# Kernel tuning notes

Hardware: AMD Instinct MI355X
Metric: run time of the kernel (lower is better)

The kernel has to match this reference:

```python
import jax, jax.numpy as jnp
import numpy as np

B, Q, D, E, V, K = 128, 32, 512, 300, 50000, 21

def kernel_mus(n):
    mus = [1.0]
    if n == 1:
        return mus
    bin_size = 2.0 / (n - 1)
    mus.append(1 - bin_size / 2)
    for i in range(1, n - 1):
        mus.append(mus[i] - bin_size)
    return mus

def kernel_sigmas(n):
    if n == 1:
        return [0.001]
    return [0.001] + [0.1] * (n - 1)

MU = jnp.asarray(kernel_mus(K), dtype=jnp.float32)        # (K,)
SIGMA = jnp.asarray(kernel_sigmas(K), dtype=jnp.float32)  # (K,)

def setup_inputs() -> dict:
    key = jax.random.key(0)
    k1, k2, k3, k4, k5, k6, k7 = jax.random.split(key, 7)
    query_idx = jax.random.randint(k1, (B, Q), 0, V)
    doc_idx = jax.random.randint(k2, (B, D), 0, V)
    query_len = jax.random.randint(k3, (B,), 1, Q + 1)
    doc_len = jax.random.randint(k4, (B,), 1, D + 1)
    emb_table = jax.random.normal(k5, (V, E), dtype=jnp.float32) * 0.1
    dense_w = jax.random.normal(k6, (1, K), dtype=jnp.float32) * 0.1
    dense_b = jax.random.normal(k7, (1,), dtype=jnp.float32) * 0.1
    return {"query_idx": query_idx, "doc_idx": doc_idx,
            "query_len": query_len, "doc_len": doc_len,
            "emb_table": emb_table, "dense_w": dense_w, "dense_b": dense_b}

def _l2norm(x):
    # F.normalize(x, p=2, dim=2): x / max(||x||, 1e-12)
    n = jnp.sqrt(jnp.sum(x * x, axis=-1, keepdims=True))
    return x / jnp.maximum(n, 1e-12)

def reference(query_idx, doc_idx, query_len, doc_len, emb_table, dense_w, dense_b):
    q_embed = _l2norm(emb_table[query_idx])   # (B,Q,E)
    d_embed = _l2norm(emb_table[doc_idx])     # (B,D,E)
    mask_q = (jnp.arange(Q)[None, :] < query_len[:, None]).astype(jnp.float32)  # (B,Q)
    mask_d = (jnp.arange(D)[None, :] < doc_len[:, None]).astype(jnp.float32)    # (B,D)
    sim = jnp.einsum('bqe,bde->bqd', q_embed, d_embed)  # (B,Q,D)
    # Gaussian kernel pooling: (B,Q,D,K) broadcast
    diff = sim[..., None] - MU
    pooling = jnp.exp(-(diff * diff) / (2.0 * SIGMA * SIGMA)) * mask_d[:, None, :, None]
    pooling_sum = jnp.sum(pooling, axis=2)                      # (B,Q,K)
    log_pool = jnp.log(jnp.clip(pooling_sum, 1e-10)) * mask_q[..., None] * 0.01
    log_pooling_sum = jnp.sum(log_pool, axis=1)                 # (B,K)
    score = jnp.squeeze(log_pooling_sum @ dense_w.T + dense_b, axis=1)  # (B,)
    return (score, log_pooling_sum)
```

## Files before the change

### kernel.cpp

```cpp
#include <hip/hip_runtime.h>

#define Bn 128
#define Qn 32
#define Dn 512
#define En 300
#define Kn 21
#define CH 32
#define JBLK 4
#define MAXIT 4
#define LDE 40
#define NKT 10
#define TILE_SH (CH * LDE)
#define BUF_SH (NKT * TILE_SH)
#define NTHR 256

typedef __attribute__((ext_vector_type(8))) short bf16x8;
typedef __attribute__((ext_vector_type(4))) float f32x4;

#define SMEM_BYTES 77440

__device__ __forceinline__ float dot4(float4 a, float4 b) {
    return a.x * b.x + a.y * b.y + a.z * b.z + a.w * b.w;
}

__global__ __launch_bounds__(NTHR, 2)
void knrm_main(const int* __restrict__ qidx, const int* __restrict__ didx,
               const int* __restrict__ dlen_arr, const float* __restrict__ table,
               float* __restrict__ partial)
{
    const int t = threadIdx.x;
    const int b = blockIdx.x >> 2;
    const int j = blockIdx.x & 3;
    const int dlen = dlen_arr[b];
    float* pbase = partial + ((size_t)(b * JBLK + j) * Qn) * Kn;

    int nc = 0;
    #pragma unroll
    for (int i = 0; i < MAXIT; ++i) if ((j + JBLK * i) * CH < dlen) nc = i + 1;

    if (nc == 0) {
        for (int i = t; i < Qn * Kn; i += NTHR) pbase[i] = 0.f;
        return;
    }

    __shared__ __align__(16) char smem[SMEM_BYTES];
    short* qbuf   = (short*)smem;
    short* dbufA  = (short*)(smem + 25600);
    short* dbufB  = (short*)(smem + 51200);
    int*   idxd   = (int*)(smem + 76800);
    int*   idxq   = idxd + MAXIT * CH;
    float* poolbf = (float*)smem;

    if (t < MAXIT * CH) {
        const int i = t >> 5, r = t & 31;
        const int doc = (j + JBLK * i) * CH + r;
        idxd[t] = (doc < dlen) ? didx[b * Dn + doc] : -1;
    } else if (t < MAXIT * CH + Qn) {
        idxq[t - MAXIT * CH] = qidx[b * Qn + (t - MAXIT * CH)];
    }
    __syncthreads();

    const int row = t >> 3;
    const int il  = t & 7;

    float4 ld[NKT];
    auto issue = [&](int tok) {
        #pragma unroll
        for (int j2 = 0; j2 < NKT; ++j2) {
            const int k = j2 * 32 + il * 4;
            float4 v = {0.f, 0.f, 0.f, 0.f};
            if (k < En && tok >= 0) v = *(const float4*)(table + (size_t)tok * En + k);
            ld[j2] = v;
        }
    };
    auto commit = [&](short* dst) {
        float ss = 0.f;
        #pragma unroll
        for (int j2 = 0; j2 < NKT; ++j2) ss += dot4(ld[j2], ld[j2]);
        ss += __shfl_xor(ss, 1);
        ss += __shfl_xor(ss, 2);
        ss += __shfl_xor(ss, 4);
        const float inv = 1.0f / fmaxf(sqrtf(ss), 1e-12f);
        #pragma unroll
        for (int j2 = 0; j2 < NKT; ++j2) {
            const unsigned ax = __float_as_uint(ld[j2].x * inv) + 0x8000u;
            const unsigned ay = __float_as_uint(ld[j2].y * inv) + 0x8000u;
            const unsigned az = __float_as_uint(ld[j2].z * inv) + 0x8000u;
            const unsigned aw = __float_as_uint(ld[j2].w * inv) + 0x8000u;
            uint2 p;
            p.x = __builtin_amdgcn_perm(ay, ax, 0x07060302u);
            p.y = __builtin_amdgcn_perm(aw, az, 0x07060302u);
            *(uint2*)&dst[j2 * TILE_SH + row * LDE + il * 4] = p;
        }
    };

    const int lane = t & 63;
    const int w = t >> 6;
    const int qt = w & 1;
    const int dt = w >> 1;
    const int frow = lane & 15;
    const int koct = lane >> 4;

    issue(idxq[row]);
    commit(qbuf);
    issue(idxd[row]);
    __syncthreads();

    bf16x8 af[NKT];
    #pragma unroll
    for (int kt = 0; kt < NKT; ++kt)
        af[kt] = *(const bf16x8*)&qbuf[kt * TILE_SH + (qt * 16 + frow) * LDE + koct * 8];

    commit(dbufA);
    __syncthreads();

    float acc[4][Kn];
    #pragma unroll
    for (int r = 0; r < 4; ++r)
        #pragma unroll
        for (int k = 0; k < Kn; ++k) acc[r][k] = 0.f;

    int p = 0;
    for (int it = 0; it < nc; ++it) {
        const bool more = (it + 1 < nc);
        if (more) issue(idxd[(it + 1) * CH + row]);

        const short* db = p ? dbufB : dbufA;
        f32x4 accS = {0.f, 0.f, 0.f, 0.f};
        #pragma unroll
        for (int kt = 0; kt < NKT; ++kt) {
            bf16x8 bf = *(const bf16x8*)&db[kt * TILE_SH + (dt * 16 + frow) * LDE + koct * 8];
            accS = __builtin_amdgcn_mfma_f32_16x16x32_bf16(af[kt], bf, accS, 0, 0, 0);
        }

        const int doc = (j + JBLK * it) * CH + dt * 16 + frow;
        if (doc < dlen) {
            #pragma unroll
            for (int r = 0; r < 4; ++r) {
                const float s = accS[r];
                #pragma unroll
                for (int k = 0; k < Kn; ++k) {
                    const float mu = (k == 0) ? 1.0f : (0.95f - 0.1f * (float)(k - 1));
                    const float cf = (k == 0) ? -500000.0f : -50.0f;
                    const float df = s - mu;
                    acc[r][k] += __expf(cf * df * df);
                }
            }
        }

        if (more) commit(p ? dbufA : dbufB);
        __syncthreads();
        p ^= 1;
    }

    #pragma unroll
    for (int r = 0; r < 4; ++r) {
        #pragma unroll
        for (int k = 0; k < Kn; ++k) poolbf[t * Kn + k] = acc[r][k];
        __syncthreads();
        for (int i = t; i < 8 * Kn; i += NTHR) {
            const int qq = i / Kn;
            const int k  = i - qq * Kn;
            const int qt2 = qq >> 2, ko2 = qq & 3;
            float s = 0.f;
            #pragma unroll
            for (int dt2 = 0; dt2 < 2; ++dt2)
                #pragma unroll
                for (int col = 0; col < 16; ++col)
                    s += poolbf[((qt2 + 2 * dt2) * 64 + ko2 * 16 + col) * Kn + k];
            pbase[(qt2 * 16 + ko2 * 4 + r) * Kn + k] = s;
        }
        __syncthreads();
    }
}

__global__ __launch_bounds__(704)
void knrm_reduce(const int* __restrict__ qlen_arr, const float* __restrict__ partial,
                 const float* __restrict__ dense_w, const float* __restrict__ dense_b,
                 float* __restrict__ out)
{
    __shared__ float sq[Qn * Kn];
    __shared__ float lk[Kn];
    const int b = blockIdx.x;
    const int t = threadIdx.x;
    const int qlen = qlen_arr[b];
    if (t < Qn * Kn) {
        const int q = t / Kn, k = t - q * Kn;
        float s = 0.f;
        #pragma unroll
        for (int c = 0; c < JBLK; ++c)
            s += partial[(((size_t)b * JBLK + c) * Qn + q) * Kn + k];
        sq[t] = (q < qlen) ? 0.01f * logf(fmaxf(s, 1e-10f)) : 0.f;
    }
    __syncthreads();
    if (t < Kn) {
        float l = 0.f;
        #pragma unroll
        for (int q = 0; q < Qn; ++q) l += sq[q * Kn + t];
        out[Bn + (size_t)b * Kn + t] = l;
        lk[t] = l;
    }
    __syncthreads();
    if (t == 0) {
        float sc = dense_b[0];
        #pragma unroll
        for (int k = 0; k < Kn; ++k) sc += lk[k] * dense_w[k];
        out[b] = sc;
    }
}

extern "C" void kernel_launch(void* const* d_in, const int* in_sizes, int n_in,
                              void* d_out, int out_size, void* d_ws, size_t ws_size,
                              hipStream_t stream)
{
    const int*   qidx  = (const int*)d_in[0];
    const int*   didx  = (const int*)d_in[1];
    const int*   qlen  = (const int*)d_in[2];
    const int*   dlen  = (const int*)d_in[3];
    const float* table = (const float*)d_in[4];
    const float* dw    = (const float*)d_in[5];
    const float* db    = (const float*)d_in[6];
    float* out = (float*)d_out;
    float* partial = (float*)d_ws;

    knrm_main<<<dim3(Bn * JBLK), dim3(NTHR), 0, stream>>>(qidx, didx, dlen, table, partial);
    knrm_reduce<<<dim3(Bn), dim3(704), 0, stream>>>(qlen, partial, dw, db, out);
}
```

Baseline: 29.59 us.

## Stage similarity tile in LDS and split kernel bins across threads

Each MFMA similarity tile is now written to shared memory. Every thread then evaluates 3 of the 21 Gaussian kernels for one query row across all 32 docs, replacing per-thread 4x21 accumulators and the end-of-kernel shared-memory reduction. The doc buffer is single-buffered and shared memory drops, so launch bounds move to 3 blocks per CU. Block indices are also swizzled across batches to balance the work. In exchange there is an extra barrier per chunk, the next-chunk load is less overlapped, and one of the eight thread groups sits idle during the exp loop.

```diff
diff --git a/kernel.cpp b/kernel.cpp
--- a/kernel.cpp
+++ b/kernel.cpp
@@ -8,48 +8,48 @@
 #define CH 32
 #define JBLK 4
 #define MAXIT 4
+#define NKT 10
 #define LDE 40
-#define NKT 10
 #define TILE_SH (CH * LDE)
-#define BUF_SH (NKT * TILE_SH)
+#define SIMLD 36
 #define NTHR 256
 
 typedef __attribute__((ext_vector_type(8))) short bf16x8;
 typedef __attribute__((ext_vector_type(4))) float f32x4;
 
-#define SMEM_BYTES 77440
+#define SMEM_BYTES 51840
 
 __device__ __forceinline__ float dot4(float4 a, float4 b) {
     return a.x * b.x + a.y * b.y + a.z * b.z + a.w * b.w;
 }
 
-__global__ __launch_bounds__(NTHR, 2)
+__global__ __launch_bounds__(NTHR, 3)
 void knrm_main(const int* __restrict__ qidx, const int* __restrict__ didx,
                const int* __restrict__ dlen_arr, const float* __restrict__ table,
                float* __restrict__ partial)
 {
+    const int g = blockIdx.x;
+    const int idx2 = (g & 7) * 64 + (g >> 3);
+    const int b = idx2 >> 2;
+    const int j = idx2 & 3;
+    const int dlen = dlen_arr[b];
+    float* pbase = partial + (size_t)(b * JBLK + j) * Qn * Kn;
+
     const int t = threadIdx.x;
-    const int b = blockIdx.x >> 2;
-    const int j = blockIdx.x & 3;
-    const int dlen = dlen_arr[b];
-    float* pbase = partial + ((size_t)(b * JBLK + j) * Qn) * Kn;
-
     int nc = 0;
     #pragma unroll
     for (int i = 0; i < MAXIT; ++i) if ((j + JBLK * i) * CH < dlen) nc = i + 1;
-
     if (nc == 0) {
         for (int i = t; i < Qn * Kn; i += NTHR) pbase[i] = 0.f;
         return;
     }
 
     __shared__ __align__(16) char smem[SMEM_BYTES];
-    short* qbuf   = (short*)smem;
-    short* dbufA  = (short*)(smem + 25600);
-    short* dbufB  = (short*)(smem + 51200);
-    int*   idxd   = (int*)(smem + 76800);
-    int*   idxq   = idxd + MAXIT * CH;
-    float* poolbf = (float*)smem;
+    short* dbuf = (short*)smem;
+    short* qbuf = (short*)(smem + 25600);
+    float* sim  = (float*)(smem + 25600);
+    int*   idxd = (int*)(smem + 51200);
+    int*   idxq = idxd + MAXIT * CH;
 
     if (t < MAXIT * CH) {
         const int i = t >> 5, r = t & 31;
@@ -69,7 +69,7 @@
         for (int j2 = 0; j2 < NKT; ++j2) {
             const int k = j2 * 32 + il * 4;
             float4 v = {0.f, 0.f, 0.f, 0.f};
-            if (k < En && tok >= 0) v = *(const float4*)(table + (size_t)tok * En + k);
+            if (k <= 296 && tok >= 0) v = *(const float4*)(table + (size_t)tok * En + k);
             ld[j2] = v;
         }
     };
@@ -96,8 +96,8 @@
 
     const int lane = t & 63;
     const int w = t >> 6;
-    const int qt = w & 1;
-    const int dt = w >> 1;
+    const int qt = w >> 1;
+    const int dt = w & 1;
     const int frow = lane & 15;
     const int koct = lane >> 4;
 
@@ -110,67 +110,61 @@
     #pragma unroll
     for (int kt = 0; kt < NKT; ++kt)
         af[kt] = *(const bf16x8*)&qbuf[kt * TILE_SH + (qt * 16 + frow) * LDE + koct * 8];
-
-    commit(dbufA);
-    __syncthreads();
-
-    float acc[4][Kn];
+    commit(dbuf);
+    __syncthreads();
+
+    const int pq = t >> 3;
+    const int kg = t & 7;
+    float mu[3], cf[3];
     #pragma unroll
-    for (int r = 0; r < 4; ++r)
-        #pragma unroll
-        for (int k = 0; k < Kn; ++k) acc[r][k] = 0.f;
-
-    int p = 0;
+    for (int kk = 0; kk < 3; ++kk) {
+        const int k = kg * 3 + kk;
+        mu[kk] = (k == 0) ? 1.0f : 1.05f - 0.1f * (float)k;
+        cf[kk] = (k == 0) ? -500000.0f : -50.0f;
+    }
+    float acc[3] = {0.f, 0.f, 0.f};
+
     for (int it = 0; it < nc; ++it) {
         const bool more = (it + 1 < nc);
         if (more) issue(idxd[(it + 1) * CH + row]);
 
-        const short* db = p ? dbufB : dbufA;
         f32x4 accS = {0.f, 0.f, 0.f, 0.f};
         #pragma unroll
         for (int kt = 0; kt < NKT; ++kt) {
-            bf16x8 bf = *(const bf16x8*)&db[kt * TILE_SH + (dt * 16 + frow) * LDE + koct * 8];
+            bf16x8 bf = *(const bf16x8*)&dbuf[kt * TILE_SH + (dt * 16 + frow) * LDE + koct * 8];
             accS = __builtin_amdgcn_mfma_f32_16x16x32_bf16(af[kt], bf, accS, 0, 0, 0);
         }
-
-        const int doc = (j + JBLK * it) * CH + dt * 16 + frow;
-        if (doc < dlen) {
+        #pragma unroll
+        for (int r = 0; r < 4; ++r)
+            sim[(qt * 16 + koct * 4 + r) * SIMLD + dt * 16 + frow] = accS[r];
+        __syncthreads();
+
+        if (more) commit(dbuf);
+
+        if (kg < 7) {
+            const int cbase = (j + JBLK * it) * CH;
             #pragma unroll
-            for (int r = 0; r < 4; ++r) {
-                const float s = accS[r];
+            for (int f4 = 0; f4 < 8; ++f4) {
+                const float4 sv = *(const float4*)&sim[pq * SIMLD + f4 * 4];
                 #pragma unroll
-                for (int k = 0; k < Kn; ++k) {
-                    const float mu = (k == 0) ? 1.0f : (0.95f - 0.1f * (float)(k - 1));
-                    const float cf = (k == 0) ? -500000.0f : -50.0f;
-                    const float df = s - mu;
-                    acc[r][k] += __expf(cf * df * df);
+                for (int e = 0; e < 4; ++e) {
+                    const float se = (e == 0) ? sv.x : (e == 1) ? sv.y : (e == 2) ? sv.z : sv.w;
+                    const float s = (cbase + f4 * 4 + e < dlen) ? se : 1.0e3f;
+                    #pragma unroll
+                    for (int kk = 0; kk < 3; ++kk) {
+                        const float d = s - mu[kk];
+                        acc[kk] += __expf(cf[kk] * d * d);
+                    }
                 }
             }
         }
-
-        if (more) commit(p ? dbufA : dbufB);
         __syncthreads();
-        p ^= 1;
-    }
-
-    #pragma unroll
-    for (int r = 0; r < 4; ++r) {
-        #pragma unroll
-        for (int k = 0; k < Kn; ++k) poolbf[t * Kn + k] = acc[r][k];
-        __syncthreads();
-        for (int i = t; i < 8 * Kn; i += NTHR) {
-            const int qq = i / Kn;
-            const int k  = i - qq * Kn;
-            const int qt2 = qq >> 2, ko2 = qq & 3;
-            float s = 0.f;
-            #pragma unroll
-            for (int dt2 = 0; dt2 < 2; ++dt2)
-                #pragma unroll
-                for (int col = 0; col < 16; ++col)
-                    s += poolbf[((qt2 + 2 * dt2) * 64 + ko2 * 16 + col) * Kn + k];
-            pbase[(qt2 * 16 + ko2 * 4 + r) * Kn + k] = s;
-        }
-        __syncthreads();
+    }
+
+    if (kg < 7) {
+        #pragma unroll
+        for (int kk = 0; kk < 3; ++kk)
+            pbase[pq * Kn + kg * 3 + kk] = acc[kk];
     }
 }
 
```

Result: faster. 26.79 us (-9.4%).
